# Optimization experiments

Measured on AMD Instinct MI355X. Metric: run time of the kernel, lower is better.

## Reference

```python
import jax, jax.numpy as jnp
import numpy as np

N_NODES = 100000


def _gcn_conv(x, row, col, W, b, num_nodes):
    """PyG GCNConv: symmetric normalization with self-loops, then linear.
    row/col already include self-loops. x: [N, d_in], W: [d_in, d_out]."""
    xw = x @ W  # [N, d_out]
    ones = jnp.ones(row.shape[0], dtype=x.dtype)
    deg = jax.ops.segment_sum(ones, col, num_segments=num_nodes)  # in-degree incl self-loop
    deg_inv_sqrt = jnp.where(deg > 0, jax.lax.rsqrt(jnp.maximum(deg, 1e-12)), 0.0)
    norm = deg_inv_sqrt[row] * deg_inv_sqrt[col]  # [E]
    msgs = xw[row] * norm[:, None]  # gather + scale, [E, d_out]
    out = jax.ops.segment_sum(msgs, col, num_segments=num_nodes)  # scatter-add
    return out + b


def _add_self_loops(edge_index, num_nodes):
    loop = jnp.arange(num_nodes, dtype=edge_index.dtype)
    row = jnp.concatenate([edge_index[0], loop])
    col = jnp.concatenate([edge_index[1], loop])
    return row, col


def setup_inputs() -> dict:
    key = jax.random.key(0)
    k_x, k_e, k_w1, k_b1, k_w2, k_b2 = jax.random.split(key, 6)
    in_dim, hidden_dim, out_dim = 64, 64, 32
    n_edges = 1600000
    x = jax.random.normal(k_x, (N_NODES, in_dim), dtype=jnp.float32)
    edge_index = jax.random.randint(k_e, (2, n_edges), 0, N_NODES, dtype=jnp.int64)
    # Glorot init like PyG's GCNConv linear weights
    s1 = float(np.sqrt(6.0 / (in_dim + hidden_dim)))
    s2 = float(np.sqrt(6.0 / (hidden_dim + out_dim)))
    W1 = jax.random.uniform(k_w1, (in_dim, hidden_dim), minval=-s1, maxval=s1, dtype=jnp.float32)
    b1 = jnp.zeros((hidden_dim,), dtype=jnp.float32)
    W2 = jax.random.uniform(k_w2, (hidden_dim, out_dim), minval=-s2, maxval=s2, dtype=jnp.float32)
    b2 = jnp.zeros((out_dim,), dtype=jnp.float32)
    return {"x": x, "edge_index": edge_index, "W1": W1, "b1": b1, "W2": W2, "b2": b2}


def reference(x, edge_index, W1, b1, W2, b2):
    row, col = _add_self_loops(edge_index, N_NODES)
    h = jax.nn.relu(_gcn_conv(x, row, col, W1, b1, N_NODES))
    out = _gcn_conv(h, row, col, W2, b2, N_NODES)
    return out
```

## Files before the change

### kernel.cpp

```cpp
#include <hip/hip_runtime.h>

#define NN 100000
#define FB_SH 10
#define FB_N  1024
#define NFB   98
#define NBLK  256
#define BH_TOT (NFB * NBLK)

static __device__ __forceinline__ unsigned short f2bf(float f) {
    unsigned u = __float_as_uint(f);
    u += 0x7fffu + ((u >> 16) & 1u);
    return (unsigned short)(u >> 16);
}
static __device__ __forceinline__ float bf2f(unsigned short h) {
    return __uint_as_float(((unsigned)h) << 16);
}


__global__ __launch_bounds__(256) void k_hist1(const int* __restrict__ coli,
                                               int* __restrict__ bhist, int E, int chunk) {
    __shared__ int h[NFB];
    for (int i = threadIdx.x; i < NFB; i += 256) h[i] = 0;
    __syncthreads();
    int bk = blockIdx.x;
    int beg = bk * chunk, end = min(E, beg + chunk);
    for (int e = beg + threadIdx.x; e < end; e += 256)
        atomicAdd(&h[coli[e] >> FB_SH], 1);
    __syncthreads();
    for (int i = threadIdx.x; i < NFB; i += 256)
        bhist[i * NBLK + bk] = h[i];
}

__global__ __launch_bounds__(1024) void k_scanA(int* __restrict__ a,
                                                int* __restrict__ blksum, int n) {
    __shared__ int sh[1024];
    int i = blockIdx.x * 1024 + threadIdx.x;
    int v = (i < n) ? a[i] : 0;
    sh[threadIdx.x] = v;
    __syncthreads();
    #pragma unroll
    for (int d = 1; d < 1024; d <<= 1) {
        int t = (threadIdx.x >= d) ? sh[threadIdx.x - d] : 0;
        __syncthreads();
        sh[threadIdx.x] += t;
        __syncthreads();
    }
    if (i < n) a[i] = sh[threadIdx.x] - v;
    if (threadIdx.x == 1023) blksum[blockIdx.x] = sh[1023];
}

__global__ void k_scanB(int* __restrict__ blksum, int nb, int* __restrict__ off, int E) {
    if (threadIdx.x == 0 && blockIdx.x == 0) {
        int s = 0;
        for (int b = 0; b < nb; ++b) { int t = blksum[b]; blksum[b] = s; s += t; }
        off[NN] = E;
    }
}

__global__ __launch_bounds__(256) void k_scanC(int* __restrict__ a,
                                               const int* __restrict__ blksum, int n) {
    int i = blockIdx.x * 256 + threadIdx.x;
    if (i < n) a[i] += blksum[i >> 10];
}

__global__ __launch_bounds__(256) void k_bin2(
    const int* __restrict__ rowi, const int* __restrict__ coli,
    const int* __restrict__ bbase, unsigned int* __restrict__ cbin, int E, int chunk)
{
    __shared__ int cur[NFB];
    int bk = blockIdx.x;
    for (int i = threadIdx.x; i < NFB; i += 256) cur[i] = bbase[i * NBLK + bk];
    __syncthreads();
    int beg = bk * chunk, end = min(E, beg + chunk);
    for (int e = beg + threadIdx.x; e < end; e += 256) {
        int col = coli[e];
        int row = rowi[e];
        int b = col >> FB_SH;
        unsigned int val = ((unsigned int)row << FB_SH) | (unsigned int)(col & (FB_N - 1));
        int pos = atomicAdd(&cur[b], 1);
        cbin[pos] = val;
    }
}

__global__ __launch_bounds__(1024) void k_csr(
    const unsigned int* __restrict__ cbin, const int* __restrict__ bbase,
    int* __restrict__ off, float* __restrict__ dinv,
    int* __restrict__ srcs, int n, int E)
{
    __shared__ int hist[FB_N];
    __shared__ int wsum[16];
    int b = blockIdx.x;
    int beg = bbase[b * NBLK];
    int end = (b + 1 < NFB) ? bbase[(b + 1) * NBLK] : E;
    int tid = threadIdx.x;
    hist[tid] = 0;
    __syncthreads();
    for (int e = beg + tid; e < end; e += 1024)
        atomicAdd(&hist[cbin[e] & (FB_N - 1)], 1);
    __syncthreads();
    int v = hist[tid];
    int lane = tid & 63;
    int wid  = tid >> 6;
    int incl = v;
    #pragma unroll
    for (int d = 1; d < 64; d <<= 1) {
        int t = __shfl_up(incl, d, 64);
        if (lane >= d) incl += t;
    }
    if (lane == 63) wsum[wid] = incl;
    __syncthreads();
    if (wid == 0) {
        int ws = (lane < 16) ? wsum[lane] : 0;
        int wincl = ws;
        #pragma unroll
        for (int d = 1; d < 16; d <<= 1) {
            int t = __shfl_up(wincl, d, 64);
            if (lane >= d) wincl += t;
        }
        if (lane < 16) wsum[lane] = wincl - ws;
    }
    __syncthreads();
    int excl = wsum[wid] + incl - v;
    int node = (b << FB_SH) + tid;
    if (node < n) {
        off[node]  = beg + excl;
        dinv[node] = rsqrtf((float)(v + 1));
    }
    __syncthreads();
    hist[tid] = excl;
    __syncthreads();
    for (int e = beg + tid; e < end; e += 1024) {
        unsigned int pv = cbin[e];
        int cl  = (int)(pv & (FB_N - 1));
        int row = (int)(pv >> FB_SH);
        int p = atomicAdd(&hist[cl], 1);
        srcs[beg + p] = row;
    }
}

template<int DOUT>
__global__ __launch_bounds__(256) void k_gemm_scale(
    const float* __restrict__ X, const float* __restrict__ W,
    const float* __restrict__ dinv, unsigned short* __restrict__ Ybf, int n)
{
    constexpr int TPR = DOUT / 4;
    constexpr int R   = 256 / TPR;
    __shared__ float sW[64 * DOUT];
    __shared__ float sX[R * 64];

    for (int i = threadIdx.x; i < 64 * DOUT; i += 256) sW[i] = W[i];
    int r0 = blockIdx.x * R;
    for (int i = threadIdx.x; i < R * 64; i += 256) {
        int r = r0 + (i >> 6);
        sX[i] = (r < n) ? X[(size_t)r * 64 + (i & 63)] : 0.0f;
    }
    __syncthreads();

    int lr  = threadIdx.x / TPR;
    int c4  = (threadIdx.x % TPR) * 4;
    int row = r0 + lr;
    const float* xr = &sX[lr * 64];
    float4 acc = make_float4(0.f, 0.f, 0.f, 0.f);
    #pragma unroll
    for (int k = 0; k < 64; ++k) {
        float xv = xr[k];
        const float* wr = &sW[k * DOUT + c4];
        acc.x = fmaf(xv, wr[0], acc.x);
        acc.y = fmaf(xv, wr[1], acc.y);
        acc.z = fmaf(xv, wr[2], acc.z);
        acc.w = fmaf(xv, wr[3], acc.w);
    }
    if (row < n) {
        float s = dinv[row];
        ushort4 o;
        o.x = f2bf(acc.x * s);
        o.y = f2bf(acc.y * s);
        o.z = f2bf(acc.z * s);
        o.w = f2bf(acc.w * s);
        *(ushort4*)&Ybf[(size_t)row * DOUT + c4] = o;
    }
}

template<bool RELU>
__global__ __launch_bounds__(256) void k_agg64(
    const unsigned short* __restrict__ Ybf, const int* __restrict__ off,
    const int* __restrict__ srcs, const float* __restrict__ dinv,
    const float* __restrict__ bias, float* __restrict__ O, int n)
{
    int node = blockIdx.x * 4 + (threadIdx.x >> 6);
    if (node >= n) return;
    int l  = threadIdx.x & 63;
    int h  = l >> 5;
    int ch = (l & 31) * 2;
    int beg = off[node], end = off[node + 1];
    float a0 = 0.f, a1 = 0.f;
    int j = beg;
    for (; j + 16 <= end; j += 16) {
        #pragma unroll
        for (int k = 0; k < 8; ++k) {
            int src = srcs[j + 2 * k + h];
            ushort2 u = *(const ushort2*)&Ybf[(size_t)src * 64 + ch];
            a0 += bf2f(u.x); a1 += bf2f(u.y);
        }
    }
    for (; j + 2 <= end; j += 2) {
        int src = srcs[j + h];
        ushort2 u = *(const ushort2*)&Ybf[(size_t)src * 64 + ch];
        a0 += bf2f(u.x); a1 += bf2f(u.y);
    }
    if (h == 0) {
        if (j < end) {
            int src = srcs[j];
            ushort2 u = *(const ushort2*)&Ybf[(size_t)src * 64 + ch];
            a0 += bf2f(u.x); a1 += bf2f(u.y);
        }
        ushort2 u = *(const ushort2*)&Ybf[(size_t)node * 64 + ch];
        a0 += bf2f(u.x); a1 += bf2f(u.y);
    }
    a0 += __shfl_xor(a0, 32, 64);
    a1 += __shfl_xor(a1, 32, 64);
    if (h == 0) {
        float d = dinv[node];
        float2 o;
        o.x = fmaf(d, a0, bias[ch]);
        o.y = fmaf(d, a1, bias[ch + 1]);
        if (RELU) { o.x = fmaxf(o.x, 0.f); o.y = fmaxf(o.y, 0.f); }
        *(float2*)&O[(size_t)node * 64 + ch] = o;
    }
}

template<bool RELU>
__global__ __launch_bounds__(256) void k_agg32(
    const unsigned short* __restrict__ Ybf, const int* __restrict__ off,
    const int* __restrict__ srcs, const float* __restrict__ dinv,
    const float* __restrict__ bias, float* __restrict__ O, int n)
{
    int node = blockIdx.x * 4 + (threadIdx.x >> 6);
    if (node >= n) return;
    int l  = threadIdx.x & 63;
    int q  = l >> 4;
    int ch = (l & 15) * 2;
    int beg = off[node], end = off[node + 1];
    float a0 = 0.f, a1 = 0.f;
    int j = beg;
    for (; j + 16 <= end; j += 16) {
        #pragma unroll
        for (int k = 0; k < 4; ++k) {
            int src = srcs[j + 4 * k + q];
            ushort2 u = *(const ushort2*)&Ybf[(size_t)src * 32 + ch];
            a0 += bf2f(u.x); a1 += bf2f(u.y);
        }
    }
    for (; j + 4 <= end; j += 4) {
        int src = srcs[j + q];
        ushort2 u = *(const ushort2*)&Ybf[(size_t)src * 32 + ch];
        a0 += bf2f(u.x); a1 += bf2f(u.y);
    }
    if (q < end - j) {
        int src = srcs[j + q];
        ushort2 u = *(const ushort2*)&Ybf[(size_t)src * 32 + ch];
        a0 += bf2f(u.x); a1 += bf2f(u.y);
    }
    if (q == 0) {
        ushort2 u = *(const ushort2*)&Ybf[(size_t)node * 32 + ch];
        a0 += bf2f(u.x); a1 += bf2f(u.y);
    }
    a0 += __shfl_xor(a0, 16, 64);
    a1 += __shfl_xor(a1, 16, 64);
    a0 += __shfl_xor(a0, 32, 64);
    a1 += __shfl_xor(a1, 32, 64);
    if (q == 0) {
        float d = dinv[node];
        float2 o;
        o.x = fmaf(d, a0, bias[ch]);
        o.y = fmaf(d, a1, bias[ch + 1]);
        if (RELU) { o.x = fmaxf(o.x, 0.f); o.y = fmaxf(o.y, 0.f); }
        *(float2*)&O[(size_t)node * 32 + ch] = o;
    }
}

extern "C" void kernel_launch(void* const* d_in, const int* in_sizes, int n_in,
                              void* d_out, int out_size, void* d_ws, size_t ws_size,
                              hipStream_t stream) {
    const float* x  = (const float*)d_in[0];
    const int*   ei = (const int*)d_in[1];
    const float* W1 = (const float*)d_in[2];
    const float* b1 = (const float*)d_in[3];
    const float* W2 = (const float*)d_in[4];
    const float* b2 = (const float*)d_in[5];
    float* out = (float*)d_out;

    const int n = NN;
    const int E = in_sizes[1] / 2;
    const int* rowi = ei;
    const int* coli = ei + E;
    const int chunk = (E + NBLK - 1) / NBLK;

    char* p = (char*)d_ws;
    auto alloc = [&p](size_t bytes) { char* q = p; p += (bytes + 255) & ~(size_t)255; return q; };
    int*   bhist  = (int*)alloc((size_t)BH_TOT * 4);
    int*   blksum = (int*)alloc(32 * 4);
    int*   off    = (int*)alloc((size_t)(n + 1) * 4);
    float* dinv   = (float*)alloc((size_t)n * 4);
    int*   srcs   = (int*)alloc((size_t)E * 4);
    unsigned short* Ybf1 = (unsigned short*)alloc((size_t)n * 64 * 2);
    unsigned short* Ybf2 = (unsigned short*)alloc((size_t)n * 32 * 2);
    float* H      = (float*)alloc((size_t)n * 64 * 4);
    unsigned int* cbin = (unsigned int*)H;

    k_hist1<<<NBLK, 256, 0, stream>>>(coli, bhist, E, chunk);
    int nbs = (BH_TOT + 1023) / 1024;
    k_scanA<<<nbs, 1024, 0, stream>>>(bhist, blksum, BH_TOT);
    k_scanB<<<1, 64, 0, stream>>>(blksum, nbs, off, E);
    k_scanC<<<(BH_TOT + 255) / 256, 256, 0, stream>>>(bhist, blksum, BH_TOT);
    k_bin2<<<NBLK, 256, 0, stream>>>(rowi, coli, bhist, cbin, E, chunk);
    k_csr<<<NFB, 1024, 0, stream>>>(cbin, bhist, off, dinv, srcs, n, E);

    k_gemm_scale<64><<<(n + 15) / 16, 256, 0, stream>>>(x, W1, dinv, Ybf1, n);
    k_agg64<true><<<(n + 3) / 4, 256, 0, stream>>>(Ybf1, off, srcs, dinv, b1, H, n);

    k_gemm_scale<32><<<(n + 31) / 32, 256, 0, stream>>>(H, W2, dinv, Ybf2, n);
    k_agg32<false><<<(n + 3) / 4, 256, 0, stream>>>(Ybf2, off, srcs, dinv, b2, out, n);
}
```

Baseline: 209.7 us.

## Split layer-1 features into two column planes mapped to separate XCD halves

The first GEMM now writes its bf16 output as two 32-column planes instead of interleaved 64-column rows. The layer-1 aggregation is rewritten to handle one plane per block, and the block index is mapped so that XCDs 0-3 gather from one plane and XCDs 4-7 from the other. Each half therefore works on a 6.4 MB table, which is meant to raise L2 hit rates for the random gathers. In exchange the grid is twice as large, so the CSR offsets and source indices are read twice, and 64-byte gathers replace 128-byte ones.

```diff
diff --git a/kernel.cpp b/kernel.cpp
--- a/kernel.cpp
+++ b/kernel.cpp
@@ -138,7 +138,7 @@
     }
 }
 
-template<int DOUT>
+template<int DOUT, bool PLANES>
 __global__ __launch_bounds__(256) void k_gemm_scale(
     const float* __restrict__ X, const float* __restrict__ W,
     const float* __restrict__ dinv, unsigned short* __restrict__ Ybf, int n)
@@ -177,55 +177,69 @@
         o.y = f2bf(acc.y * s);
         o.z = f2bf(acc.z * s);
         o.w = f2bf(acc.w * s);
-        *(ushort4*)&Ybf[(size_t)row * DOUT + c4] = o;
+        if (PLANES) {
+            constexpr int HC = DOUT / 2;
+            int plane = c4 / HC;
+            int cw    = c4 % HC;
+            *(ushort4*)&Ybf[(size_t)plane * n * HC + (size_t)row * HC + cw] = o;
+        } else {
+            *(ushort4*)&Ybf[(size_t)row * DOUT + c4] = o;
+        }
     }
 }
 
 template<bool RELU>
-__global__ __launch_bounds__(256) void k_agg64(
-    const unsigned short* __restrict__ Ybf, const int* __restrict__ off,
+__global__ __launch_bounds__(256) void k_agg64s(
+    const unsigned short* __restrict__ Yp, const int* __restrict__ off,
     const int* __restrict__ srcs, const float* __restrict__ dinv,
     const float* __restrict__ bias, float* __restrict__ O, int n)
 {
-    int node = blockIdx.x * 4 + (threadIdx.x >> 6);
+    int xcd  = blockIdx.x & 7;
+    int half = xcd >> 2;
+    int quad = (blockIdx.x >> 3) * 4 + (xcd & 3);
+    int node = quad * 4 + (threadIdx.x >> 6);
     if (node >= n) return;
+    const unsigned short* P = Yp + (size_t)half * n * 32;
     int l  = threadIdx.x & 63;
-    int h  = l >> 5;
-    int ch = (l & 31) * 2;
+    int q  = l >> 4;
+    int ch = (l & 15) * 2;
     int beg = off[node], end = off[node + 1];
     float a0 = 0.f, a1 = 0.f;
     int j = beg;
     for (; j + 16 <= end; j += 16) {
         #pragma unroll
-        for (int k = 0; k < 8; ++k) {
-            int src = srcs[j + 2 * k + h];
-            ushort2 u = *(const ushort2*)&Ybf[(size_t)src * 64 + ch];
+        for (int k = 0; k < 4; ++k) {
+            int src = srcs[j + 4 * k + q];
+            ushort2 u = *(const ushort2*)&P[(size_t)src * 32 + ch];
             a0 += bf2f(u.x); a1 += bf2f(u.y);
         }
     }
-    for (; j + 2 <= end; j += 2) {
-        int src = srcs[j + h];
-        ushort2 u = *(const ushort2*)&Ybf[(size_t)src * 64 + ch];
-        a0 += bf2f(u.x); a1 += bf2f(u.y);
-    }
-    if (h == 0) {
-        if (j < end) {
-            int src = srcs[j];
-            ushort2 u = *(const ushort2*)&Ybf[(size_t)src * 64 + ch];
-            a0 += bf2f(u.x); a1 += bf2f(u.y);
-        }
-        ushort2 u = *(const ushort2*)&Ybf[(size_t)node * 64 + ch];
-        a0 += bf2f(u.x); a1 += bf2f(u.y);
-    }
+    for (; j + 4 <= end; j += 4) {
+        int src = srcs[j + q];
+        ushort2 u = *(const ushort2*)&P[(size_t)src * 32 + ch];
+        a0 += bf2f(u.x); a1 += bf2f(u.y);
+    }
+    if (q < end - j) {
+        int src = srcs[j + q];
+        ushort2 u = *(const ushort2*)&P[(size_t)src * 32 + ch];
+        a0 += bf2f(u.x); a1 += bf2f(u.y);
+    }
+    if (q == 0) {
+        ushort2 u = *(const ushort2*)&P[(size_t)node * 32 + ch];
+        a0 += bf2f(u.x); a1 += bf2f(u.y);
+    }
+    a0 += __shfl_xor(a0, 16, 64);
+    a1 += __shfl_xor(a1, 16, 64);
     a0 += __shfl_xor(a0, 32, 64);
     a1 += __shfl_xor(a1, 32, 64);
-    if (h == 0) {
+    if (q == 0) {
         float d = dinv[node];
+        int cg = half * 32 + ch;
         float2 o;
-        o.x = fmaf(d, a0, bias[ch]);
-        o.y = fmaf(d, a1, bias[ch + 1]);
+        o.x = fmaf(d, a0, bias[cg]);
+        o.y = fmaf(d, a1, bias[cg + 1]);
         if (RELU) { o.x = fmaxf(o.x, 0.f); o.y = fmaxf(o.y, 0.f); }
-        *(float2*)&O[(size_t)node * 64 + ch] = o;
+        *(float2*)&O[(size_t)node * 64 + cg] = o;
     }
 }
 
@@ -316,9 +330,11 @@
     k_bin2<<<NBLK, 256, 0, stream>>>(rowi, coli, bhist, cbin, E, chunk);
     k_csr<<<NFB, 1024, 0, stream>>>(cbin, bhist, off, dinv, srcs, n, E);
 
-    k_gemm_scale<64><<<(n + 15) / 16, 256, 0, stream>>>(x, W1, dinv, Ybf1, n);
-    k_agg64<true><<<(n + 3) / 4, 256, 0, stream>>>(Ybf1, off, srcs, dinv, b1, H, n);
-
-    k_gemm_scale<32><<<(n + 31) / 32, 256, 0, stream>>>(H, W2, dinv, Ybf2, n);
+    k_gemm_scale<64, true><<<(n + 15) / 16, 256, 0, stream>>>(x, W1, dinv, Ybf1, n);
+    int nq = (n + 3) / 4;
+    int nb64 = ((2 * nq + 7) / 8) * 8;
+    k_agg64s<true><<<nb64, 256, 0, stream>>>(Ybf1, off, srcs, dinv, b1, H, n);
+
+    k_gemm_scale<32, false><<<(n + 31) / 32, 256, 0, stream>>>(H, W2, dinv, Ybf2, n);
     k_agg32<false><<<(n + 3) / 4, 256, 0, stream>>>(Ybf2, off, srcs, dinv, b2, out, n);
 }
```

New measurement: 232.3 us. +10.8%, slower.

## Split layer-1 features into channel quarters with XCC-affine work-stealing aggregation

Applied to the files above, without the earlier changes.

The first GEMM now writes its bf16 output as four planes of 16 channels each, so each plane is a quarter of the table size and has a better chance of staying resident in the L2 of one XCD. The layer-1 aggregation becomes a persistent kernel that takes 256-node work items from per-quarter atomic counters. Each block starts on the quarter chosen by its XCC ID, and each wave gathers 8 edges at a time with 16 channels per edge. In exchange, every node's CSR row is read four times, each gather moves only 32 bytes, and the atomic ticket loop adds block-level syncs.

```diff
diff --git a/kernel.cpp b/kernel.cpp
--- a/kernel.cpp
+++ b/kernel.cpp
@@ -6,6 +6,8 @@
 #define NFB   98
 #define NBLK  256
 #define BH_TOT (NFB * NBLK)
+#define ITEM_NODES 256
+#define NITEMS ((NN + ITEM_NODES - 1) / ITEM_NODES)
 
 static __device__ __forceinline__ unsigned short f2bf(float f) {
     unsigned u = __float_as_uint(f);
@@ -138,7 +140,7 @@
     }
 }
 
-template<int DOUT>
+template<int DOUT, bool QUARTERS>
 __global__ __launch_bounds__(256) void k_gemm_scale(
     const float* __restrict__ X, const float* __restrict__ W,
     const float* __restrict__ dinv, unsigned short* __restrict__ Ybf, int n)
@@ -177,55 +179,87 @@
         o.y = f2bf(acc.y * s);
         o.z = f2bf(acc.z * s);
         o.w = f2bf(acc.w * s);
-        *(ushort4*)&Ybf[(size_t)row * DOUT + c4] = o;
+        if (QUARTERS) {
+            int qp = c4 >> 4;
+            int cw = c4 & 15;
+            *(ushort4*)&Ybf[(size_t)qp * n * 16 + (size_t)row * 16 + cw] = o;
+        } else {
+            *(ushort4*)&Ybf[(size_t)row * DOUT + c4] = o;
+        }
     }
 }
 
 template<bool RELU>
-__global__ __launch_bounds__(256) void k_agg64(
-    const unsigned short* __restrict__ Ybf, const int* __restrict__ off,
+__global__ __launch_bounds__(256) void k_agg64q(
+    const unsigned short* __restrict__ Yq, const int* __restrict__ off,
     const int* __restrict__ srcs, const float* __restrict__ dinv,
-    const float* __restrict__ bias, float* __restrict__ O, int n)
-{
-    int node = blockIdx.x * 4 + (threadIdx.x >> 6);
-    if (node >= n) return;
-    int l  = threadIdx.x & 63;
-    int h  = l >> 5;
-    int ch = (l & 31) * 2;
-    int beg = off[node], end = off[node + 1];
-    float a0 = 0.f, a1 = 0.f;
-    int j = beg;
-    for (; j + 16 <= end; j += 16) {
-        #pragma unroll
-        for (int k = 0; k < 8; ++k) {
-            int src = srcs[j + 2 * k + h];
-            ushort2 u = *(const ushort2*)&Ybf[(size_t)src * 64 + ch];
-            a0 += bf2f(u.x); a1 += bf2f(u.y);
+    const float* __restrict__ bias, float* __restrict__ O, int n,
+    int* __restrict__ cur)
+{
+    __shared__ int s_ticket;
+    unsigned xcc;
+    asm volatile("s_getreg_b32 %0, hwreg(HW_REG_XCC_ID)" : "=s"(xcc));
+    int pref = (xcc >> 1) & 3;
+    int wid  = threadIdx.x >> 6;
+    int l    = threadIdx.x & 63;
+    int slot = l >> 3;
+    int ch   = (l & 7) * 2;
+
+    for (int dq = 0; dq < 4; ++dq) {
+        int q = (pref + dq) & 3;
+        const unsigned short* P = Yq + (size_t)q * n * 16;
+        int cgl = q * 16 + ch;
+        float b0 = bias[cgl], b1 = bias[cgl + 1];
+        while (true) {
+            if (threadIdx.x == 0) s_ticket = atomicAdd(&cur[q], 1);
+            __syncthreads();
+            int t = s_ticket;
+            __syncthreads();
+            if (t >= NITEMS) break;
+            int r0 = t * ITEM_NODES + wid * (ITEM_NODES / 4);
+            int r1 = min(n, r0 + ITEM_NODES / 4);
+            for (int node = r0; node < r1; ++node) {
+                int beg = off[node], end = off[node + 1];
+                float a0 = 0.f, a1 = 0.f;
+                int j = beg;
+                for (; j + 16 <= end; j += 16) {
+                    int s1i = srcs[j + slot];
+                    int s2i = srcs[j + 8 + slot];
+                    ushort2 u1 = *(const ushort2*)&P[(size_t)s1i * 16 + ch];
+                    ushort2 u2 = *(const ushort2*)&P[(size_t)s2i * 16 + ch];
+                    a0 += bf2f(u1.x); a1 += bf2f(u1.y);
+                    a0 += bf2f(u2.x); a1 += bf2f(u2.y);
+                }
+                for (; j + 8 <= end; j += 8) {
+                    int si = srcs[j + slot];
+                    ushort2 u = *(const ushort2*)&P[(size_t)si * 16 + ch];
+                    a0 += bf2f(u.x); a1 += bf2f(u.y);
+                }
+                if (slot < end - j) {
+                    int si = srcs[j + slot];
+                    ushort2 u = *(const ushort2*)&P[(size_t)si * 16 + ch];
+                    a0 += bf2f(u.x); a1 += bf2f(u.y);
+                }
+                if (slot == 0) {
+                    ushort2 u = *(const ushort2*)&P[(size_t)node * 16 + ch];
+                    a0 += bf2f(u.x); a1 += bf2f(u.y);
+                }
+                a0 += __shfl_xor(a0, 8, 64);
+                a1 += __shfl_xor(a1, 8, 64);
+                a0 += __shfl_xor(a0, 16, 64);
+                a1 += __shfl_xor(a1, 16, 64);
+                a0 += __shfl_xor(a0, 32, 64);
+                a1 += __shfl_xor(a1, 32, 64);
+                if (slot == 0) {
+                    float d = dinv[node];
+                    float2 o;
+                    o.x = fmaf(d, a0, b0);
+                    o.y = fmaf(d, a1, b1);
+                    if (RELU) { o.x = fmaxf(o.x, 0.f); o.y = fmaxf(o.y, 0.f); }
+                    *(float2*)&O[(size_t)node * 64 + cgl] = o;
+                }
+            }
         }
-    }
-    for (; j + 2 <= end; j += 2) {
-        int src = srcs[j + h];
-        ushort2 u = *(const ushort2*)&Ybf[(size_t)src * 64 + ch];
-        a0 += bf2f(u.x); a1 += bf2f(u.y);
-    }
-    if (h == 0) {
-        if (j < end) {
-            int src = srcs[j];
-            ushort2 u = *(const ushort2*)&Ybf[(size_t)src * 64 + ch];
-            a0 += bf2f(u.x); a1 += bf2f(u.y);
-        }
-        ushort2 u = *(const ushort2*)&Ybf[(size_t)node * 64 + ch];
-        a0 += bf2f(u.x); a1 += bf2f(u.y);
-    }
-    a0 += __shfl_xor(a0, 32, 64);
-    a1 += __shfl_xor(a1, 32, 64);
-    if (h == 0) {
-        float d = dinv[node];
-        float2 o;
-        o.x = fmaf(d, a0, bias[ch]);
-        o.y = fmaf(d, a1, bias[ch + 1]);
-        if (RELU) { o.x = fmaxf(o.x, 0.f); o.y = fmaxf(o.y, 0.f); }
-        *(float2*)&O[(size_t)node * 64 + ch] = o;
     }
 }
 
@@ -300,10 +334,11 @@
     auto alloc = [&p](size_t bytes) { char* q = p; p += (bytes + 255) & ~(size_t)255; return q; };
     int*   bhist  = (int*)alloc((size_t)BH_TOT * 4);
     int*   blksum = (int*)alloc(32 * 4);
+    int*   qcur   = (int*)alloc(256);
     int*   off    = (int*)alloc((size_t)(n + 1) * 4);
     float* dinv   = (float*)alloc((size_t)n * 4);
     int*   srcs   = (int*)alloc((size_t)E * 4);
-    unsigned short* Ybf1 = (unsigned short*)alloc((size_t)n * 64 * 2);
+    unsigned short* Yq1  = (unsigned short*)alloc((size_t)n * 64 * 2);
     unsigned short* Ybf2 = (unsigned short*)alloc((size_t)n * 32 * 2);
     float* H      = (float*)alloc((size_t)n * 64 * 4);
     unsigned int* cbin = (unsigned int*)H;
@@ -316,9 +351,10 @@
     k_bin2<<<NBLK, 256, 0, stream>>>(rowi, coli, bhist, cbin, E, chunk);
     k_csr<<<NFB, 1024, 0, stream>>>(cbin, bhist, off, dinv, srcs, n, E);
 
-    k_gemm_scale<64><<<(n + 15) / 16, 256, 0, stream>>>(x, W1, dinv, Ybf1, n);
-    k_agg64<true><<<(n + 3) / 4, 256, 0, stream>>>(Ybf1, off, srcs, dinv, b1, H, n);
-
-    k_gemm_scale<32><<<(n + 31) / 32, 256, 0, stream>>>(H, W2, dinv, Ybf2, n);
+    hipMemsetAsync(qcur, 0, 16, stream);
+    k_gemm_scale<64, true><<<(n + 15) / 16, 256, 0, stream>>>(x, W1, dinv, Yq1, n);
+    k_agg64q<true><<<1024, 256, 0, stream>>>(Yq1, off, srcs, dinv, b1, H, n, qcur);
+
+    k_gemm_scale<32, false><<<(n + 31) / 32, 256, 0, stream>>>(H, W2, dinv, Ybf2, n);
     k_agg32<false><<<(n + 3) / 4, 256, 0, stream>>>(Ybf2, off, srcs, dinv, b2, out, n);
 }
```

Measured after the change: 405.4 us. 93.3% more time.

## Store hidden layer as bf16, vectorize GEMM loads, fuse scan kernels

Applied to the files above, without the earlier changes.

The hidden activation H written by the first aggregation is now stored as bf16 rather than fp32, and the second GEMM reads it as bf16, halving that round trip through memory. The GEMM staging loads for W and X now use float4/ushort4 vector loads. The single-thread scanB kernel is folded into scanC, where each block recomputes the small block-sum prefix in shared memory, removing one launch. The bf16 hidden layer adds rounding error to the second layer's input.

```diff
diff --git a/kernel.cpp b/kernel.cpp
--- a/kernel.cpp
+++ b/kernel.cpp
@@ -1,4 +1,5 @@
 #include <hip/hip_runtime.h>
+#include <type_traits>
 
 #define NN 100000
 #define FB_SH 10
@@ -49,18 +50,21 @@
     if (threadIdx.x == 1023) blksum[blockIdx.x] = sh[1023];
 }
 
-__global__ void k_scanB(int* __restrict__ blksum, int nb, int* __restrict__ off, int E) {
-    if (threadIdx.x == 0 && blockIdx.x == 0) {
+__global__ __launch_bounds__(256) void k_scanC(int* __restrict__ a,
+                                               const int* __restrict__ blksum,
+                                               int nbs, int n,
+                                               int* __restrict__ off, int E) {
+    __shared__ int pre[32];
+    if (threadIdx.x < 32) pre[threadIdx.x] = (threadIdx.x < nbs) ? blksum[threadIdx.x] : 0;
+    __syncthreads();
+    if (threadIdx.x == 0) {
         int s = 0;
-        for (int b = 0; b < nb; ++b) { int t = blksum[b]; blksum[b] = s; s += t; }
-        off[NN] = E;
-    }
-}
-
-__global__ __launch_bounds__(256) void k_scanC(int* __restrict__ a,
-                                               const int* __restrict__ blksum, int n) {
+        for (int b = 0; b < nbs; ++b) { int t = pre[b]; pre[b] = s; s += t; }
+    }
+    __syncthreads();
     int i = blockIdx.x * 256 + threadIdx.x;
-    if (i < n) a[i] += blksum[i >> 10];
+    if (i < n) a[i] += pre[i >> 10];
+    if (i == 0) off[NN] = E;
 }
 
 __global__ __launch_bounds__(256) void k_bin2(
@@ -138,9 +142,9 @@
     }
 }
 
-template<int DOUT>
+template<int DOUT, typename TIN>
 __global__ __launch_bounds__(256) void k_gemm_scale(
-    const float* __restrict__ X, const float* __restrict__ W,
+    const TIN* __restrict__ X, const float* __restrict__ W,
     const float* __restrict__ dinv, unsigned short* __restrict__ Ybf, int n)
 {
     constexpr int TPR = DOUT / 4;
@@ -148,11 +152,23 @@
     __shared__ float sW[64 * DOUT];
     __shared__ float sX[R * 64];
 
-    for (int i = threadIdx.x; i < 64 * DOUT; i += 256) sW[i] = W[i];
+    for (int i = threadIdx.x; i < 16 * DOUT; i += 256)
+        *(float4*)&sW[i * 4] = *(const float4*)&W[i * 4];
     int r0 = blockIdx.x * R;
-    for (int i = threadIdx.x; i < R * 64; i += 256) {
-        int r = r0 + (i >> 6);
-        sX[i] = (r < n) ? X[(size_t)r * 64 + (i & 63)] : 0.0f;
+    for (int i = threadIdx.x; i < R * 16; i += 256) {
+        int lr  = i >> 4;
+        int c4i = (i & 15) * 4;
+        int r = r0 + lr;
+        float4 v;
+        if (r < n) {
+            if constexpr (std::is_same<TIN, float>::value) {
+                v = *(const float4*)&X[(size_t)r * 64 + c4i];
+            } else {
+                ushort4 u = *(const ushort4*)&X[(size_t)r * 64 + c4i];
+                v = make_float4(bf2f(u.x), bf2f(u.y), bf2f(u.z), bf2f(u.w));
+            }
+        } else v = make_float4(0.f, 0.f, 0.f, 0.f);
+        *(float4*)&sX[lr * 64 + c4i] = v;
     }
     __syncthreads();
 
@@ -181,11 +197,10 @@
     }
 }
 
-template<bool RELU>
 __global__ __launch_bounds__(256) void k_agg64(
     const unsigned short* __restrict__ Ybf, const int* __restrict__ off,
     const int* __restrict__ srcs, const float* __restrict__ dinv,
-    const float* __restrict__ bias, float* __restrict__ O, int n)
+    const float* __restrict__ bias, unsigned short* __restrict__ O, int n)
 {
     int node = blockIdx.x * 4 + (threadIdx.x >> 6);
     if (node >= n) return;
@@ -221,15 +236,15 @@
     a1 += __shfl_xor(a1, 32, 64);
     if (h == 0) {
         float d = dinv[node];
-        float2 o;
-        o.x = fmaf(d, a0, bias[ch]);
-        o.y = fmaf(d, a1, bias[ch + 1]);
-        if (RELU) { o.x = fmaxf(o.x, 0.f); o.y = fmaxf(o.y, 0.f); }
-        *(float2*)&O[(size_t)node * 64 + ch] = o;
-    }
-}
-
-template<bool RELU>
+        float o0 = fmaxf(fmaf(d, a0, bias[ch]),     0.f);
+        float o1 = fmaxf(fmaf(d, a1, bias[ch + 1]), 0.f);
+        ushort2 o;
+        o.x = f2bf(o0);
+        o.y = f2bf(o1);
+        *(ushort2*)&O[(size_t)node * 64 + ch] = o;
+    }
+}
+
 __global__ __launch_bounds__(256) void k_agg32(
     const unsigned short* __restrict__ Ybf, const int* __restrict__ off,
     const int* __restrict__ srcs, const float* __restrict__ dinv,
@@ -274,7 +289,6 @@
         float2 o;
         o.x = fmaf(d, a0, bias[ch]);
         o.y = fmaf(d, a1, bias[ch + 1]);
-        if (RELU) { o.x = fmaxf(o.x, 0.f); o.y = fmaxf(o.y, 0.f); }
         *(float2*)&O[(size_t)node * 32 + ch] = o;
     }
 }
@@ -305,20 +319,19 @@
     int*   srcs   = (int*)alloc((size_t)E * 4);
     unsigned short* Ybf1 = (unsigned short*)alloc((size_t)n * 64 * 2);
     unsigned short* Ybf2 = (unsigned short*)alloc((size_t)n * 32 * 2);
-    float* H      = (float*)alloc((size_t)n * 64 * 4);
-    unsigned int* cbin = (unsigned int*)H;
+    unsigned short* Hbf  = (unsigned short*)alloc((size_t)n * 64 * 2);
+    unsigned int* cbin = (unsigned int*)Hbf;
 
     k_hist1<<<NBLK, 256, 0, stream>>>(coli, bhist, E, chunk);
     int nbs = (BH_TOT + 1023) / 1024;
     k_scanA<<<nbs, 1024, 0, stream>>>(bhist, blksum, BH_TOT);
-    k_scanB<<<1, 64, 0, stream>>>(blksum, nbs, off, E);
-    k_scanC<<<(BH_TOT + 255) / 256, 256, 0, stream>>>(bhist, blksum, BH_TOT);
+    k_scanC<<<(BH_TOT + 255) / 256, 256, 0, stream>>>(bhist, blksum, nbs, BH_TOT, off, E);
     k_bin2<<<NBLK, 256, 0, stream>>>(rowi, coli, bhist, cbin, E, chunk);
     k_csr<<<NFB, 1024, 0, stream>>>(cbin, bhist, off, dinv, srcs, n, E);
 
-    k_gemm_scale<64><<<(n + 15) / 16, 256, 0, stream>>>(x, W1, dinv, Ybf1, n);
-    k_agg64<true><<<(n + 3) / 4, 256, 0, stream>>>(Ybf1, off, srcs, dinv, b1, H, n);
-
-    k_gemm_scale<32><<<(n + 31) / 32, 256, 0, stream>>>(H, W2, dinv, Ybf2, n);
-    k_agg32<false><<<(n + 3) / 4, 256, 0, stream>>>(Ybf2, off, srcs, dinv, b2, out, n);
-}
+    k_gemm_scale<64, float><<<(n + 15) / 16, 256, 0, stream>>>(x, W1, dinv, Ybf1, n);
+    k_agg64<<<(n + 3) / 4, 256, 0, stream>>>(Ybf1, off, srcs, dinv, b1, Hbf, n);
+
+    k_gemm_scale<32, unsigned short><<<(n + 31) / 32, 256, 0, stream>>>(Hbf, W2, dinv, Ybf2, n);
+    k_agg32<<<(n + 3) / 4, 256, 0, stream>>>(Ybf2, off, srcs, dinv, b2, out, n);
+}
```

Result: faster. 197.6 us (-5.8%).
